# Kernel optimization log

Hardware: AMD Instinct MI355X
Metric: run time of the kernel (lower is better)

## Reference

```python
import jax, jax.numpy as jnp
import numpy as np

S = 30.0  # scale
M = 0.5   # angular margin

N, D, C = 1024, 512, 100000


def setup_inputs() -> dict:
    key = jax.random.key(0)
    k1, k2, k3 = jax.random.split(key, 3)
    embeddings = jax.random.normal(k1, (N, D), dtype=jnp.float32)
    weight = jax.random.normal(k2, (C, D), dtype=jnp.float32)
    labels = jax.random.randint(k3, (N,), 0, C, dtype=jnp.int64)
    return {"embeddings": embeddings, "weight": weight, "labels": labels}


def _l2norm(x, axis=-1, eps=1e-12):
    # matches torch F.normalize: x / max(||x||, eps)
    n = jnp.sqrt(jnp.sum(x * x, axis=axis, keepdims=True))
    return x / jnp.maximum(n, eps)


def reference(embeddings, weight, labels):
    e = _l2norm(embeddings)                      # [N, D]
    w = _l2norm(weight)                          # [C, D]
    cos_theta = jnp.clip(e @ w.T, -1.0, 1.0)     # [N, C]
    theta = jnp.arccos(cos_theta)
    cos_theta_m = jnp.cos(theta + M)
    # apply margin only at the label-indexed entry per row (one-hot blend)
    rows = jnp.arange(cos_theta.shape[0])
    target_vals = cos_theta_m[rows, labels]
    logits = cos_theta.at[rows, labels].set(target_vals)
    return S * logits
```

## Files before the change

### kernel.cpp

```cpp
#include <hip/hip_runtime.h>
#include <cstdint>
#include <cstddef>


constexpr int N_ROWS  = 1024;
constexpr int DIM     = 512;
constexpr int C_CLS   = 100000;
constexpr int NPANEL  = 392;
constexpr int MTILES  = 8;

#define COS_M 0.87758256189037271612f
#define SIN_M 0.47942553860420300027f

typedef __attribute__((ext_vector_type(8))) __bf16 bf16x8;
typedef __attribute__((ext_vector_type(4))) float  floatx4;

__device__ inline unsigned short f2bf(float f) {
    unsigned int u = __float_as_uint(f);
    u += 0x7FFFu + ((u >> 16) & 1u);
    return (unsigned short)(u >> 16);
}

__device__ inline float wave_reduce_sum(float v) {
    v += __shfl_xor(v, 32, 64);
    v += __shfl_xor(v, 16, 64);
    v += __shfl_xor(v, 8, 64);
    v += __shfl_xor(v, 4, 64);
    v += __shfl_xor(v, 2, 64);
    v += __shfl_xor(v, 1, 64);
    return v;
}

__device__ inline void async16(const void* g, void* l) {
    __builtin_amdgcn_global_load_lds(
        (const __attribute__((address_space(1))) void*)g,
        (__attribute__((address_space(3))) void*)l,
        16, 0, 0);
}

__global__ __launch_bounds__(256) void normalize_rows(
    const float* __restrict__ in, unsigned short* __restrict__ out, int rows) {
    int wave = (int)((blockIdx.x * 256u + threadIdx.x) >> 6);
    int lane = threadIdx.x & 63;
    if (wave >= rows) return;

    const float4* rp = (const float4*)(in + (size_t)wave * DIM);
    float4 x0 = rp[lane];
    float4 x1 = rp[64 + lane];
    float s = x0.x*x0.x + x0.y*x0.y + x0.z*x0.z + x0.w*x0.w
            + x1.x*x1.x + x1.y*x1.y + x1.z*x1.z + x1.w*x1.w;
    s = wave_reduce_sum(s);
    float inv = 1.0f / fmaxf(sqrtf(s), 1e-12f);
    unsigned short* orow = out + (size_t)wave * DIM;
    ushort4 o0, o1;
    o0.x = f2bf(x0.x * inv); o0.y = f2bf(x0.y * inv);
    o0.z = f2bf(x0.z * inv); o0.w = f2bf(x0.w * inv);
    o1.x = f2bf(x1.x * inv); o1.y = f2bf(x1.y * inv);
    o1.z = f2bf(x1.z * inv); o1.w = f2bf(x1.w * inv);
    ((ushort4*)orow)[lane]      = o0;
    ((ushort4*)orow)[64 + lane] = o1;
}

__global__ __launch_bounds__(512, 4) void arcface_gemm(
    const unsigned short* __restrict__ A,
    const unsigned short* __restrict__ Wn,
    const int* __restrict__ labels,
    float* __restrict__ out) {
    __shared__ unsigned short Asm[2][4096];
    __shared__ unsigned short Bsm[2][8192];
    __shared__ int labs[128];

    const int tid  = threadIdx.x;
    const int lane = tid & 63;
    const int wv   = tid >> 6;
    const int wr   = wv >> 2;
    const int wc   = wv & 3;
    const int mrow = lane & 15;

    const int bid   = blockIdx.x;
    const int xcd   = bid & 7;
    const int s     = bid >> 3;
    const int panel = xcd * (NPANEL / 8) + (s >> 3);
    const int mtile = s & 7;
    const int mbase = mtile * 128;
    const int nbase = panel * 256;

    if (tid < 128) labs[tid] = labels[mbase + tid];

    const int sg    = tid >> 6;
    const int smrow = lane & 15;
    const int skq   = lane >> 4;
    const unsigned short* aSrc = A + (size_t)(mbase + sg * 16 + smrow) * DIM + skq * 8;
    int brow0 = nbase + sg * 16 + smrow;
    int brow1 = nbase + 128 + sg * 16 + smrow;
    if (brow0 > C_CLS - 1) brow0 = C_CLS - 1;
    if (brow1 > C_CLS - 1) brow1 = C_CLS - 1;
    const unsigned short* bSrc0 = Wn + (size_t)brow0 * DIM + skq * 8;
    const unsigned short* bSrc1 = Wn + (size_t)brow1 * DIM + skq * 8;

    #define STAGE(buf, k0)                                         \
        do {                                                       \
            async16(aSrc  + (k0), &Asm[buf][tid * 8]);             \
            async16(bSrc0 + (k0), &Bsm[buf][tid * 8]);             \
            async16(bSrc1 + (k0), &Bsm[buf][4096 + tid * 8]);      \
        } while (0)

    floatx4 acc[4][4];
    #pragma unroll
    for (int i = 0; i < 4; i++)
        #pragma unroll
        for (int j = 0; j < 4; j++)
            acc[i][j] = (floatx4){0.f, 0.f, 0.f, 0.f};

    const int aoff = wr * 2048 + lane * 8;
    const int boff = wc * 2048 + lane * 8;

    STAGE(0, 0);
    __syncthreads();

    int cur = 0;
    for (int t = 0; t < 15; t++) {
        STAGE(cur ^ 1, (t + 1) * 32);
        bf16x8 af[4], bfr[4];
        #pragma unroll
        for (int i = 0; i < 4; i++)
            af[i] = *(const bf16x8*)&Asm[cur][aoff + i * 512];
        #pragma unroll
        for (int j = 0; j < 4; j++)
            bfr[j] = *(const bf16x8*)&Bsm[cur][boff + j * 512];
        #pragma unroll
        for (int i = 0; i < 4; i++)
            #pragma unroll
            for (int j = 0; j < 4; j++)
                acc[i][j] = __builtin_amdgcn_mfma_f32_16x16x32_bf16(
                    af[i], bfr[j], acc[i][j], 0, 0, 0);
        __syncthreads();
        cur ^= 1;
    }
    {
        bf16x8 af[4], bfr[4];
        #pragma unroll
        for (int i = 0; i < 4; i++)
            af[i] = *(const bf16x8*)&Asm[cur][aoff + i * 512];
        #pragma unroll
        for (int j = 0; j < 4; j++)
            bfr[j] = *(const bf16x8*)&Bsm[cur][boff + j * 512];
        #pragma unroll
        for (int i = 0; i < 4; i++)
            #pragma unroll
            for (int j = 0; j < 4; j++)
                acc[i][j] = __builtin_amdgcn_mfma_f32_16x16x32_bf16(
                    af[i], bfr[j], acc[i][j], 0, 0, 0);
    }

    const int col0 = nbase + wc * 64 + mrow;
    #pragma unroll
    for (int i = 0; i < 4; i++) {
        const int rbase = wr * 64 + i * 16 + (lane >> 4) * 4;
        #pragma unroll
        for (int r = 0; r < 4; r++) {
            const int row  = rbase + r;
            const int grow = mbase + row;
            const int lab  = labs[row];
            float* orow = out + (size_t)grow * C_CLS;
            #pragma unroll
            for (int j = 0; j < 4; j++) {
                const int gc = col0 + j * 16;
                if (gc < C_CLS) {
                    float c = acc[i][j][r];
                    c = fminf(1.0f, fmaxf(-1.0f, c));
                    float v = c;
                    if (gc == lab) {
                        v = COS_M * c - SIN_M * sqrtf(fmaxf(0.0f, 1.0f - c * c));
                    }
                    orow[gc] = 30.0f * v;
                }
            }
        }
    }
    #undef STAGE
}

extern "C" void kernel_launch(void* const* d_in, const int* in_sizes, int n_in,
                              void* d_out, int out_size, void* d_ws, size_t ws_size,
                              hipStream_t stream) {
    const float* emb    = (const float*)d_in[0];
    const float* wgt    = (const float*)d_in[1];
    const int*   labels = (const int*)d_in[2];
    float*       out    = (float*)d_out;

    unsigned short* An = (unsigned short*)d_ws;
    unsigned short* Wn = (unsigned short*)((char*)d_ws + (size_t)N_ROWS * DIM * 2);

    normalize_rows<<<N_ROWS / 4, 256, 0, stream>>>(emb, An, N_ROWS);
    normalize_rows<<<C_CLS / 4, 256, 0, stream>>>(wgt, Wn, C_CLS);
    arcface_gemm<<<dim3(MTILES * NPANEL), 512, 0, stream>>>(An, Wn, labels, out);
}
```

Baseline: 758.0 us.

## Triple-buffer LDS staging with manual vmcnt waits and MFMA priority boost

Moves the GEMM main loop from double to triple buffering. Two K-slices are prefetched ahead, and the full __syncthreads is replaced with explicit s_waitcnt vmcnt(3) plus s_barrier, so global-to-LDS loads overlap more with MFMA work. s_setprio is raised around the MFMA block to favor the compute waves. The cost is 50% more LDS per block, which may lower occupancy, and hand-written waitcnt counts that must stay correct.

```diff
diff --git a/kernel.cpp b/kernel.cpp
--- a/kernel.cpp
+++ b/kernel.cpp
@@ -66,8 +66,8 @@
     const unsigned short* __restrict__ Wn,
     const int* __restrict__ labels,
     float* __restrict__ out) {
-    __shared__ unsigned short Asm[2][4096];
-    __shared__ unsigned short Bsm[2][8192];
+    __shared__ unsigned short Asm[3][4096];
+    __shared__ unsigned short Bsm[3][8192];
     __shared__ int labs[128];
 
     const int tid  = threadIdx.x;
@@ -115,43 +115,42 @@
     const int aoff = wr * 2048 + lane * 8;
     const int boff = wc * 2048 + lane * 8;
 
+    #define COMPUTE(buf)                                                      \
+        do {                                                                  \
+            bf16x8 af[4], bfr[4];                                             \
+            _Pragma("unroll")                                                 \
+            for (int i = 0; i < 4; i++)                                       \
+                af[i] = *(const bf16x8*)&Asm[buf][aoff + i * 512];            \
+            _Pragma("unroll")                                                 \
+            for (int j = 0; j < 4; j++)                                       \
+                bfr[j] = *(const bf16x8*)&Bsm[buf][boff + j * 512];           \
+            __builtin_amdgcn_s_setprio(1);                                    \
+            _Pragma("unroll")                                                 \
+            for (int i = 0; i < 4; i++)                                       \
+                _Pragma("unroll")                                             \
+                for (int j = 0; j < 4; j++)                                   \
+                    acc[i][j] = __builtin_amdgcn_mfma_f32_16x16x32_bf16(      \
+                        af[i], bfr[j], acc[i][j], 0, 0, 0);                   \
+            __builtin_amdgcn_s_setprio(0);                                    \
+        } while (0)
+
     STAGE(0, 0);
-    __syncthreads();
+    STAGE(1, 32);
+    asm volatile("s_waitcnt lgkmcnt(0)" ::: "memory");
 
-    int cur = 0;
-    for (int t = 0; t < 15; t++) {
-        STAGE(cur ^ 1, (t + 1) * 32);
-        bf16x8 af[4], bfr[4];
-        #pragma unroll
-        for (int i = 0; i < 4; i++)
-            af[i] = *(const bf16x8*)&Asm[cur][aoff + i * 512];
-        #pragma unroll
-        for (int j = 0; j < 4; j++)
-            bfr[j] = *(const bf16x8*)&Bsm[cur][boff + j * 512];
-        #pragma unroll
-        for (int i = 0; i < 4; i++)
-            #pragma unroll
-            for (int j = 0; j < 4; j++)
-                acc[i][j] = __builtin_amdgcn_mfma_f32_16x16x32_bf16(
-                    af[i], bfr[j], acc[i][j], 0, 0, 0);
-        __syncthreads();
-        cur ^= 1;
+    #pragma unroll
+    for (int t = 0; t < 14; t++) {
+        asm volatile("s_waitcnt vmcnt(3)" ::: "memory");
+        asm volatile("s_barrier" ::: "memory");
+        STAGE((t + 2) % 3, (t + 2) * 32);
+        COMPUTE(t % 3);
     }
-    {
-        bf16x8 af[4], bfr[4];
-        #pragma unroll
-        for (int i = 0; i < 4; i++)
-            af[i] = *(const bf16x8*)&Asm[cur][aoff + i * 512];
-        #pragma unroll
-        for (int j = 0; j < 4; j++)
-            bfr[j] = *(const bf16x8*)&Bsm[cur][boff + j * 512];
-        #pragma unroll
-        for (int i = 0; i < 4; i++)
-            #pragma unroll
-            for (int j = 0; j < 4; j++)
-                acc[i][j] = __builtin_amdgcn_mfma_f32_16x16x32_bf16(
-                    af[i], bfr[j], acc[i][j], 0, 0, 0);
-    }
+    asm volatile("s_waitcnt vmcnt(3)" ::: "memory");
+    asm volatile("s_barrier" ::: "memory");
+    COMPUTE(2);
+    asm volatile("s_waitcnt vmcnt(0)" ::: "memory");
+    asm volatile("s_barrier" ::: "memory");
+    COMPUTE(0);
 
     const int col0 = nbase + wc * 64 + mrow;
     #pragma unroll
@@ -179,6 +178,7 @@
         }
     }
     #undef STAGE
+    #undef COMPUTE
 }
 
 extern "C" void kernel_launch(void* const* d_in, const int* in_sizes, int n_in,
```

Measured after the change: 739.7 us. 1.02x faster.
